# Kernel optimization log

Measured on AMD Instinct MI355X. Metric: run time of the kernel, lower is better.

The kernel has to match this reference:

```python
import jax, jax.numpy as jnp
import numpy as np

N = 8192
D = 256

def setup_inputs() -> dict:
    key = jax.random.key(0)
    k1, k2, k3 = jax.random.split(key, 3)
    x = jax.random.normal(k1, (N, D), dtype=jnp.float32)
    adj_matrix = jax.random.uniform(k2, (N, N), dtype=jnp.float32)
    weight = jax.random.normal(k3, (D, D), dtype=jnp.float32) * 0.02
    bias = jnp.zeros((D,), dtype=jnp.float32)
    return {"x": x, "adj_matrix": adj_matrix, "weight": weight, "bias": bias}

def reference(x, adj_matrix, weight, bias):
    # degree = row sums of adjacency
    degree = jnp.sum(adj_matrix, axis=1)  # [N]
    inv_deg = 1.0 / degree               # inverse of diagonal degree matrix
    # D^-1 @ A @ D^-1 == A scaled by inv_deg on rows and columns
    normalized_adj = adj_matrix * inv_deg[:, None] * inv_deg[None, :]  # [N,N]
    h = jnp.matmul(normalized_adj, x)          # [N,D] aggregation
    h = jnp.matmul(h, weight) + bias           # [N,D] transform
    return jax.nn.relu(h)
```

## Files before the change

### kernel.cpp

```cpp
#include <hip/hip_runtime.h>
#include <stdint.h>
#include <stdio.h>

#define NROWS 8192
#define DDIM 256

typedef __attribute__((ext_vector_type(8))) __bf16 bf16x8;
typedef __attribute__((ext_vector_type(4))) float f32x4;
typedef __attribute__((address_space(3))) uint32_t as3u32;
typedef __attribute__((address_space(1))) uint32_t as1u32;

__device__ __forceinline__ void glds16(const void* g, void* l) {
  __builtin_amdgcn_global_load_lds((const as1u32*)g, (as3u32*)l, 16, 0, 0);
}

__device__ __forceinline__ ushort f2b(float f) {
  uint32_t u = __float_as_uint(f);
  return (ushort)((u + 0x7FFFu + ((u >> 16) & 1u)) >> 16);
}

__global__ __launch_bounds__(256) void degree_kernel(const float* __restrict__ A,
                                                     float* __restrict__ inv_deg) {
  const int row = blockIdx.x * 4 + (threadIdx.x >> 6);
  const int lane = threadIdx.x & 63;
  const float4* r4 = (const float4*)(A + (size_t)row * NROWS);
  float s = 0.f;
#pragma unroll
  for (int i = 0; i < 32; ++i) {
    float4 v = r4[lane + (i << 6)];
    s += (v.x + v.y) + (v.z + v.w);
  }
#pragma unroll
  for (int o = 32; o > 0; o >>= 1) s += __shfl_xor(s, o, 64);
  if (lane == 0) inv_deg[row] = 1.0f / s;
}

__global__ __launch_bounds__(256) void transpose_scale_kernel(const float* __restrict__ src,
                                                              const float* __restrict__ scale,
                                                              ushort* __restrict__ dst, int K) {
  __shared__ ushort tile[64 * 256];
  const int k0 = blockIdx.x * 64;
  const int w = threadIdx.x >> 6;
  const int lane = threadIdx.x & 63;
#pragma unroll
  for (int i = 0; i < 16; ++i) {
    const int r = w * 16 + i;
    float4 v = *(const float4*)(src + (size_t)(k0 + r) * DDIM + lane * 4);
    const float sc = scale ? scale[k0 + r] : 1.0f;
    ushort4 b;
    b.x = f2b(v.x * sc); b.y = f2b(v.y * sc);
    b.z = f2b(v.z * sc); b.w = f2b(v.w * sc);
    *(ushort4*)&tile[r * 256 + lane * 4] = b;
  }
  __syncthreads();
  const int c = threadIdx.x;
  ushort* drow = dst + (size_t)c * K + k0;
#pragma unroll
  for (int s = 0; s < 8; ++s) {
    uint32_t p[4];
#pragma unroll
    for (int j = 0; j < 4; ++j) {
      uint32_t lo = tile[(s * 8 + 2 * j + 0) * 256 + c];
      uint32_t hi = tile[(s * 8 + 2 * j + 1) * 256 + c];
      p[j] = lo | (hi << 16);
    }
    uint4 u; u.x = p[0]; u.y = p[1]; u.z = p[2]; u.w = p[3];
    *(uint4*)(drow + s * 8) = u;
  }
}

__global__ __launch_bounds__(512, 4) void gemm_bf16_kernel(
    const float* __restrict__ Am, const float* __restrict__ Am2, int lda,
    const ushort* __restrict__ Bt, int K, int klen, int nsplit,
    const float* __restrict__ rowscale, const float* __restrict__ bias,
    int do_relu, float* __restrict__ C) {
  __shared__ ushort Asm[2][32 * 32];
  __shared__ ushort Bsm[2][256 * 32];

  const int tid = threadIdx.x;
  const int lane = tid & 63;
  const int w = tid >> 6;

  int ks, mb;
  if (nsplit == 2) { ks = blockIdx.x & 1; mb = blockIdx.x >> 1; }
  else             { ks = 0;             mb = blockIdx.x; }
  const int kstart = ks * klen;
  const int m0 = mb * 32;
  float* Cp = C + (size_t)ks * ((size_t)NROWS * DDIM);

  f32x4 acc[2][2] = {};
  const int NT = klen >> 5;

  const int arow = tid >> 3;
  const int aseg = tid & 7;
  const float* ag  = Am  + (size_t)(m0 + arow) * lda + kstart + aseg * 4;
  const float* ag2 = Am2 ? (Am2 + (size_t)(m0 + arow) * lda + kstart + aseg * 4) : nullptr;
  const int awoff = arow * 32 + ((((aseg >> 1) ^ ((arow >> 1) & 3)) << 3) | ((aseg & 1) << 2));

  const int bch0 = w * 2;
  const int bq = lane >> 2;
  const int bswz = (lane & 3) ^ ((lane >> 3) & 3);
  const char* bg0 = (const char*)Bt + (size_t)(bch0 * 16 + bq) * ((size_t)K * 2)
                    + (size_t)kstart * 2 + bswz * 16;
  const char* bg1 = bg0 + (size_t)16 * ((size_t)K * 2);

  const int fr = lane & 15;
  const int fsw = (fr >> 1) & 3;
  const int fch = (lane >> 4) ^ fsw;
  const int aoff0 = (fr) * 32 + (fch << 3);
  const int aoff1 = (16 + fr) * 32 + (fch << 3);
  const int boff0 = (w * 32 + fr) * 32 + (fch << 3);
  const int boff1 = (w * 32 + 16 + fr) * 32 + (fch << 3);

  if (tid < 256) {
    float4 v = *(const float4*)ag;
    if (ag2) { float4 v2 = *(const float4*)ag2; v.x += v2.x; v.y += v2.y; v.z += v2.z; v.w += v2.w; }
    ushort4 b; b.x = f2b(v.x); b.y = f2b(v.y); b.z = f2b(v.z); b.w = f2b(v.w);
    *(ushort4*)&Asm[0][awoff] = b;
  }
  glds16(bg0, &Bsm[0][(bch0 + 0) * 512]);
  glds16(bg1, &Bsm[0][(bch0 + 1) * 512]);

  int cur = 0;
  for (int t = 0; t < NT; ++t) {
    __syncthreads();
    const bool pf = (t + 1 < NT);
    float4 av, av2;
    if (pf) {
      if (tid < 256) {
        av = *(const float4*)(ag + (t + 1) * 32);
        if (ag2) av2 = *(const float4*)(ag2 + (t + 1) * 32);
      }
      glds16(bg0 + (size_t)(t + 1) * 64, &Bsm[cur ^ 1][(bch0 + 0) * 512]);
      glds16(bg1 + (size_t)(t + 1) * 64, &Bsm[cur ^ 1][(bch0 + 1) * 512]);
    }

    uint4 a0 = *(const uint4*)&Asm[cur][aoff0];
    uint4 a1 = *(const uint4*)&Asm[cur][aoff1];
    uint4 b0 = *(const uint4*)&Bsm[cur][boff0];
    uint4 b1 = *(const uint4*)&Bsm[cur][boff1];
    bf16x8 fa0 = __builtin_bit_cast(bf16x8, a0);
    bf16x8 fa1 = __builtin_bit_cast(bf16x8, a1);
    bf16x8 fb0 = __builtin_bit_cast(bf16x8, b0);
    bf16x8 fb1 = __builtin_bit_cast(bf16x8, b1);
    acc[0][0] = __builtin_amdgcn_mfma_f32_16x16x32_bf16(fa0, fb0, acc[0][0], 0, 0, 0);
    acc[0][1] = __builtin_amdgcn_mfma_f32_16x16x32_bf16(fa0, fb1, acc[0][1], 0, 0, 0);
    acc[1][0] = __builtin_amdgcn_mfma_f32_16x16x32_bf16(fa1, fb0, acc[1][0], 0, 0, 0);
    acc[1][1] = __builtin_amdgcn_mfma_f32_16x16x32_bf16(fa1, fb1, acc[1][1], 0, 0, 0);

    if (pf && tid < 256) {
      float4 v = av;
      if (ag2) { v.x += av2.x; v.y += av2.y; v.z += av2.z; v.w += av2.w; }
      ushort4 b; b.x = f2b(v.x); b.y = f2b(v.y); b.z = f2b(v.z); b.w = f2b(v.w);
      *(ushort4*)&Asm[cur ^ 1][awoff] = b;
    }
    cur ^= 1;
  }

#pragma unroll
  for (int m = 0; m < 2; ++m)
#pragma unroll
    for (int n = 0; n < 2; ++n) {
      const int col = w * 32 + n * 16 + fr;
      const float bv = bias ? bias[col] : 0.f;
#pragma unroll
      for (int r = 0; r < 4; ++r) {
        const int row = m0 + m * 16 + (lane >> 4) * 4 + r;
        float x = acc[m][n][r];
        if (rowscale) x *= rowscale[row];
        x += bv;
        if (do_relu) x = fmaxf(x, 0.f);
        Cp[(size_t)row * DDIM + col] = x;
      }
    }
}

extern "C" void kernel_launch(void* const* d_in, const int* in_sizes, int n_in,
                              void* d_out, int out_size, void* d_ws, size_t ws_size,
                              hipStream_t stream) {
  const float* x      = (const float*)d_in[0];
  const float* adj    = (const float*)d_in[1];
  const float* weight = (const float*)d_in[2];
  const float* bias   = (const float*)d_in[3];
  float* out = (float*)d_out;

  char* ws = (char*)d_ws;
  const size_t h_bytes  = 2ull * NROWS * DDIM * 4;
  const size_t yt_bytes = (size_t)DDIM * NROWS * 2;
  const size_t wt_bytes = (size_t)DDIM * DDIM * 2;
  float*  h       = (float*)ws;
  ushort* Yt      = (ushort*)(ws + h_bytes);
  ushort* Wt      = (ushort*)(ws + h_bytes + yt_bytes);
  float*  inv_deg = (float*)(ws + h_bytes + yt_bytes + wt_bytes);
  const size_t need = h_bytes + yt_bytes + wt_bytes + (size_t)NROWS * 4;
  if (ws_size < need) { fprintf(stderr, "ws too small: %zu < %zu\n", ws_size, need); return; }

  degree_kernel<<<NROWS / 4, 256, 0, stream>>>(adj, inv_deg);
  transpose_scale_kernel<<<NROWS / 64, 256, 0, stream>>>(x, inv_deg, Yt, NROWS);
  transpose_scale_kernel<<<DDIM / 64, 256, 0, stream>>>(weight, nullptr, Wt, DDIM);
  gemm_bf16_kernel<<<dim3(512), 512, 0, stream>>>(adj, nullptr, NROWS, Yt, NROWS,
                                                  NROWS / 2, 2, inv_deg, nullptr, 0, h);
  gemm_bf16_kernel<<<dim3(256), 512, 0, stream>>>(h, h + (size_t)NROWS * DDIM, DDIM, Wt, DDIM,
                                                  DDIM, 1, nullptr, bias, 1, out);
}
```

Before: 510.5 us.

## Pre-cast adjacency to bf16 during degree pass and use larger-tile split-K GEMM

The degree kernel now also writes a bf16 copy of the adjacency matrix. This lets the big aggregation GEMM load both operands with direct global-to-LDS loads into 128x256x64 tiles, split four ways over K, with 16 MFMAs per wave per k-step. The goal is to replace the small 32-row fp32-converting tile with a high-reuse MFMA-bound tile. In exchange it adds a 128MB bf16 write plus a read-back, and four fp32 partial outputs that the small GEMM has to sum.

```diff
diff --git a/kernel.cpp b/kernel.cpp
--- a/kernel.cpp
+++ b/kernel.cpp
@@ -19,16 +19,21 @@
   return (ushort)((u + 0x7FFFu + ((u >> 16) & 1u)) >> 16);
 }
 
-__global__ __launch_bounds__(256) void degree_kernel(const float* __restrict__ A,
-                                                     float* __restrict__ inv_deg) {
+__global__ __launch_bounds__(256) void degree_cast_kernel(const float* __restrict__ A,
+                                                          ushort* __restrict__ Ab,
+                                                          float* __restrict__ inv_deg) {
   const int row = blockIdx.x * 4 + (threadIdx.x >> 6);
   const int lane = threadIdx.x & 63;
   const float4* r4 = (const float4*)(A + (size_t)row * NROWS);
+  ushort* wr = Ab + (size_t)row * NROWS;
   float s = 0.f;
 #pragma unroll
   for (int i = 0; i < 32; ++i) {
     float4 v = r4[lane + (i << 6)];
     s += (v.x + v.y) + (v.z + v.w);
+    ushort4 b;
+    b.x = f2b(v.x); b.y = f2b(v.y); b.z = f2b(v.z); b.w = f2b(v.w);
+    *(ushort4*)(wr + (size_t)(lane + (i << 6)) * 4) = b;
   }
 #pragma unroll
   for (int o = 32; o > 0; o >>= 1) s += __shfl_xor(s, o, 64);
@@ -69,52 +74,141 @@
   }
 }
 
-__global__ __launch_bounds__(512, 4) void gemm_bf16_kernel(
-    const float* __restrict__ Am, const float* __restrict__ Am2, int lda,
-    const ushort* __restrict__ Bt, int K, int klen, int nsplit,
-    const float* __restrict__ rowscale, const float* __restrict__ bias,
-    int do_relu, float* __restrict__ C) {
-  __shared__ ushort Asm[2][32 * 32];
-  __shared__ ushort Bsm[2][256 * 32];
+__global__ __launch_bounds__(512, 2) void gemm_big_kernel(
+    const ushort* __restrict__ Ab,
+    const ushort* __restrict__ Bt,
+    const float* __restrict__ rowscale,
+    float* __restrict__ Cpart) {
+  __shared__ ushort Asm[2][128 * 64];
+  __shared__ ushort Bsm[2][256 * 64];
 
   const int tid = threadIdx.x;
   const int lane = tid & 63;
   const int w = tid >> 6;
-
-  int ks, mb;
-  if (nsplit == 2) { ks = blockIdx.x & 1; mb = blockIdx.x >> 1; }
-  else             { ks = 0;             mb = blockIdx.x; }
-  const int kstart = ks * klen;
-  const int m0 = mb * 32;
-  float* Cp = C + (size_t)ks * ((size_t)NROWS * DDIM);
+  const int wm = w >> 2;
+  const int wn = w & 3;
+
+  const int ks = blockIdx.x & 3;
+  const int mb = blockIdx.x >> 2;
+  const int m0 = mb * 128;
+  const size_t kstart = (size_t)ks * 2048;
+
+  const int al_r = lane >> 3;
+  const int al_c = lane & 7;
+  const int asw = al_c ^ al_r;
+  const char* agA = (const char*)(Ab + (size_t)(m0 + 16 * w + al_r) * NROWS + kstart) + asw * 16;
+  const char* bgB = (const char*)(Bt + (size_t)(32 * w + al_r) * NROWS + kstart) + asw * 16;
+  const size_t grp = (size_t)8 * NROWS * 2;
+
+  const int fr = lane & 15;
+  const int q = lane >> 4;
+  const int fsw = fr & 7;
+
+  f32x4 acc[4][4] = {};
+  const int NT = 2048 / 64;
+
+  {
+    glds16(agA, &Asm[0][(16 * w + 0) * 64]);
+    glds16(agA + grp, &Asm[0][(16 * w + 8) * 64]);
+#pragma unroll
+    for (int j = 0; j < 4; ++j)
+      glds16(bgB + (size_t)j * grp, &Bsm[0][(32 * w + 8 * j) * 64]);
+  }
+
+  int cur = 0;
+  for (int t = 0; t < NT; ++t) {
+    __syncthreads();
+    if (t + 1 < NT) {
+      const size_t koff = (size_t)(t + 1) * 128;
+      glds16(agA + koff, &Asm[cur ^ 1][(16 * w + 0) * 64]);
+      glds16(agA + grp + koff, &Asm[cur ^ 1][(16 * w + 8) * 64]);
+#pragma unroll
+      for (int j = 0; j < 4; ++j)
+        glds16(bgB + (size_t)j * grp + koff, &Bsm[cur ^ 1][(32 * w + 8 * j) * 64]);
+    }
+#pragma unroll
+    for (int kk = 0; kk < 2; ++kk) {
+      uint4 af[4], bfr[4];
+#pragma unroll
+      for (int m = 0; m < 4; ++m)
+        af[m] = *(const uint4*)((const char*)&Asm[cur][0] +
+                 ((64 * wm + 16 * m + fr) * 128 + (((4 * kk + q) ^ fsw) << 4)));
+#pragma unroll
+      for (int n = 0; n < 4; ++n)
+        bfr[n] = *(const uint4*)((const char*)&Bsm[cur][0] +
+                 ((64 * wn + 16 * n + fr) * 128 + (((4 * kk + q) ^ fsw) << 4)));
+#pragma unroll
+      for (int m = 0; m < 4; ++m)
+#pragma unroll
+        for (int n = 0; n < 4; ++n)
+          acc[m][n] = __builtin_amdgcn_mfma_f32_16x16x32_bf16(
+              __builtin_bit_cast(bf16x8, af[m]), __builtin_bit_cast(bf16x8, bfr[n]),
+              acc[m][n], 0, 0, 0);
+    }
+    cur ^= 1;
+  }
+
+  float* Cp = Cpart + (size_t)ks * ((size_t)NROWS * DDIM);
+#pragma unroll
+  for (int m = 0; m < 4; ++m)
+#pragma unroll
+    for (int r = 0; r < 4; ++r) {
+      const int row = m0 + 64 * wm + 16 * m + q * 4 + r;
+      const float sc = rowscale[row];
+#pragma unroll
+      for (int n = 0; n < 4; ++n) {
+        const int col = 64 * wn + 16 * n + fr;
+        Cp[(size_t)row * DDIM + col] = acc[m][n][r] * sc;
+      }
+    }
+}
+
+__global__ __launch_bounds__(512, 4) void gemm_small_kernel(
+    const float* __restrict__ Hp, int npart, size_t pstride,
+    const ushort* __restrict__ Bt,
+    const float* __restrict__ bias, float* __restrict__ C) {
+  const int K = DDIM;
+  __shared__ ushort Asm[2][32 * 32];
+  __shared__ ushort Bsm[2][256 * 32];
+
+  const int tid = threadIdx.x;
+  const int lane = tid & 63;
+  const int w = tid >> 6;
+  const int m0 = blockIdx.x * 32;
 
   f32x4 acc[2][2] = {};
-  const int NT = klen >> 5;
+  const int NT = K >> 5;
 
   const int arow = tid >> 3;
   const int aseg = tid & 7;
-  const float* ag  = Am  + (size_t)(m0 + arow) * lda + kstart + aseg * 4;
-  const float* ag2 = Am2 ? (Am2 + (size_t)(m0 + arow) * lda + kstart + aseg * 4) : nullptr;
+  const float* ag = Hp + (size_t)(m0 + arow) * DDIM + aseg * 4;
   const int awoff = arow * 32 + ((((aseg >> 1) ^ ((arow >> 1) & 3)) << 3) | ((aseg & 1) << 2));
 
   const int bch0 = w * 2;
   const int bq = lane >> 2;
   const int bswz = (lane & 3) ^ ((lane >> 3) & 3);
-  const char* bg0 = (const char*)Bt + (size_t)(bch0 * 16 + bq) * ((size_t)K * 2)
-                    + (size_t)kstart * 2 + bswz * 16;
+  const char* bg0 = (const char*)Bt + (size_t)(bch0 * 16 + bq) * ((size_t)K * 2) + bswz * 16;
   const char* bg1 = bg0 + (size_t)16 * ((size_t)K * 2);
 
   const int fr = lane & 15;
   const int fsw = (fr >> 1) & 3;
   const int fch = (lane >> 4) ^ fsw;
-  const int aoff0 = (fr) * 32 + (fch << 3);
+  const int aoff0 = fr * 32 + (fch << 3);
   const int aoff1 = (16 + fr) * 32 + (fch << 3);
   const int boff0 = (w * 32 + fr) * 32 + (fch << 3);
   const int boff1 = (w * 32 + 16 + fr) * 32 + (fch << 3);
 
+  auto loadA = [&](int t) {
+    float4 v; v.x = v.y = v.z = v.w = 0.f;
+    for (int p = 0; p < npart; ++p) {
+      float4 u = *(const float4*)(ag + (size_t)p * pstride + t * 32);
+      v.x += u.x; v.y += u.y; v.z += u.z; v.w += u.w;
+    }
+    return v;
+  };
+
   if (tid < 256) {
-    float4 v = *(const float4*)ag;
-    if (ag2) { float4 v2 = *(const float4*)ag2; v.x += v2.x; v.y += v2.y; v.z += v2.z; v.w += v2.w; }
+    float4 v = loadA(0);
     ushort4 b; b.x = f2b(v.x); b.y = f2b(v.y); b.z = f2b(v.z); b.w = f2b(v.w);
     *(ushort4*)&Asm[0][awoff] = b;
   }
@@ -125,33 +219,26 @@
   for (int t = 0; t < NT; ++t) {
     __syncthreads();
     const bool pf = (t + 1 < NT);
-    float4 av, av2;
+    float4 av;
     if (pf) {
-      if (tid < 256) {
-        av = *(const float4*)(ag + (t + 1) * 32);
-        if (ag2) av2 = *(const float4*)(ag2 + (t + 1) * 32);
-      }
+      if (tid < 256) av = loadA(t + 1);
       glds16(bg0 + (size_t)(t + 1) * 64, &Bsm[cur ^ 1][(bch0 + 0) * 512]);
       glds16(bg1 + (size_t)(t + 1) * 64, &Bsm[cur ^ 1][(bch0 + 1) * 512]);
     }
-
     uint4 a0 = *(const uint4*)&Asm[cur][aoff0];
     uint4 a1 = *(const uint4*)&Asm[cur][aoff1];
     uint4 b0 = *(const uint4*)&Bsm[cur][boff0];
     uint4 b1 = *(const uint4*)&Bsm[cur][boff1];
-    bf16x8 fa0 = __builtin_bit_cast(bf16x8, a0);
-    bf16x8 fa1 = __builtin_bit_cast(bf16x8, a1);
-    bf16x8 fb0 = __builtin_bit_cast(bf16x8, b0);
-    bf16x8 fb1 = __builtin_bit_cast(bf16x8, b1);
-    acc[0][0] = __builtin_amdgcn_mfma_f32_16x16x32_bf16(fa0, fb0, acc[0][0], 0, 0, 0);
-    acc[0][1] = __builtin_amdgcn_mfma_f32_16x16x32_bf16(fa0, fb1, acc[0][1], 0, 0, 0);
-    acc[1][0] = __builtin_amdgcn_mfma_f32_16x16x32_bf16(fa1, fb0, acc[1][0], 0, 0, 0);
-    acc[1][1] = __builtin_amdgcn_mfma_f32_16x16x32_bf16(fa1, fb1, acc[1][1], 0, 0, 0);
-
+    acc[0][0] = __builtin_amdgcn_mfma_f32_16x16x32_bf16(
+        __builtin_bit_cast(bf16x8, a0), __builtin_bit_cast(bf16x8, b0), acc[0][0], 0, 0, 0);
+    acc[0][1] = __builtin_amdgcn_mfma_f32_16x16x32_bf16(
+        __builtin_bit_cast(bf16x8, a0), __builtin_bit_cast(bf16x8, b1), acc[0][1], 0, 0, 0);
+    acc[1][0] = __builtin_amdgcn_mfma_f32_16x16x32_bf16(
+        __builtin_bit_cast(bf16x8, a1), __builtin_bit_cast(bf16x8, b0), acc[1][0], 0, 0, 0);
+    acc[1][1] = __builtin_amdgcn_mfma_f32_16x16x32_bf16(
+        __builtin_bit_cast(bf16x8, a1), __builtin_bit_cast(bf16x8, b1), acc[1][1], 0, 0, 0);
     if (pf && tid < 256) {
-      float4 v = av;
-      if (ag2) { v.x += av2.x; v.y += av2.y; v.z += av2.z; v.w += av2.w; }
-      ushort4 b; b.x = f2b(v.x); b.y = f2b(v.y); b.z = f2b(v.z); b.w = f2b(v.w);
+      ushort4 b; b.x = f2b(av.x); b.y = f2b(av.y); b.z = f2b(av.z); b.w = f2b(av.w);
       *(ushort4*)&Asm[cur ^ 1][awoff] = b;
     }
     cur ^= 1;
@@ -162,15 +249,13 @@
 #pragma unroll
     for (int n = 0; n < 2; ++n) {
       const int col = w * 32 + n * 16 + fr;
-      const float bv = bias ? bias[col] : 0.f;
+      const float bv = bias[col];
 #pragma unroll
       for (int r = 0; r < 4; ++r) {
         const int row = m0 + m * 16 + (lane >> 4) * 4 + r;
-        float x = acc[m][n][r];
-        if (rowscale) x *= rowscale[row];
-        x += bv;
-        if (do_relu) x = fmaxf(x, 0.f);
-        Cp[(size_t)row * DDIM + col] = x;
+        float x = acc[m][n][r] + bv;
+        x = fmaxf(x, 0.f);
+        C[(size_t)row * DDIM + col] = x;
       }
     }
 }
@@ -185,21 +270,21 @@
   float* out = (float*)d_out;
 
   char* ws = (char*)d_ws;
-  const size_t h_bytes  = 2ull * NROWS * DDIM * 4;
+  const size_t ab_bytes = (size_t)NROWS * NROWS * 2;
+  const size_t h_bytes  = 4ull * NROWS * DDIM * 4;
   const size_t yt_bytes = (size_t)DDIM * NROWS * 2;
   const size_t wt_bytes = (size_t)DDIM * DDIM * 2;
-  float*  h       = (float*)ws;
-  ushort* Yt      = (ushort*)(ws + h_bytes);
-  ushort* Wt      = (ushort*)(ws + h_bytes + yt_bytes);
-  float*  inv_deg = (float*)(ws + h_bytes + yt_bytes + wt_bytes);
-  const size_t need = h_bytes + yt_bytes + wt_bytes + (size_t)NROWS * 4;
+  ushort* Ab      = (ushort*)ws;
+  float*  hpart   = (float*)(ws + ab_bytes);
+  ushort* Yt      = (ushort*)(ws + ab_bytes + h_bytes);
+  ushort* Wt      = (ushort*)(ws + ab_bytes + h_bytes + yt_bytes);
+  float*  inv_deg = (float*)(ws + ab_bytes + h_bytes + yt_bytes + wt_bytes);
+  const size_t need = ab_bytes + h_bytes + yt_bytes + wt_bytes + (size_t)NROWS * 4;
   if (ws_size < need) { fprintf(stderr, "ws too small: %zu < %zu\n", ws_size, need); return; }
 
-  degree_kernel<<<NROWS / 4, 256, 0, stream>>>(adj, inv_deg);
+  degree_cast_kernel<<<NROWS / 4, 256, 0, stream>>>(adj, Ab, inv_deg);
   transpose_scale_kernel<<<NROWS / 64, 256, 0, stream>>>(x, inv_deg, Yt, NROWS);
   transpose_scale_kernel<<<DDIM / 64, 256, 0, stream>>>(weight, nullptr, Wt, DDIM);
-  gemm_bf16_kernel<<<dim3(512), 512, 0, stream>>>(adj, nullptr, NROWS, Yt, NROWS,
-                                                  NROWS / 2, 2, inv_deg, nullptr, 0, h);
-  gemm_bf16_kernel<<<dim3(256), 512, 0, stream>>>(h, h + (size_t)NROWS * DDIM, DDIM, Wt, DDIM,
-                                                  DDIM, 1, nullptr, bias, 1, out);
-}
+  gemm_big_kernel<<<dim3(256), 512, 0, stream>>>(Ab, Yt, inv_deg, hpart);
+  gemm_small_kernel<<<dim3(256), 512, 0, stream>>>(hpart, 4, (size_t)NROWS * DDIM, Wt, bias, out);
+}
```

Result: faster. 472.1 us (-7.5%).
